# Optimization experiments

Measured on AMD Instinct MI355X. Metric: run time of the kernel, lower is better.

## Reference

```python
import jax, jax.numpy as jnp
import numpy as np

B, S, HID = 1, 4096, 768
NH, HD = 12, 64  # num heads, head dim


def setup_inputs() -> dict:
    key = jax.random.key(0)
    ks = jax.random.split(key, 7)
    scale = 1.0 / np.sqrt(HID)
    return {
        "hidden_states": jax.random.normal(ks[0], (B, S, HID), dtype=jnp.float32),
        "attention_mask": jnp.zeros((B, 1, 1, S), dtype=jnp.float32),
        "Wq": jax.random.normal(ks[1], (HID, HID), dtype=jnp.float32) * scale,
        "bq": jnp.zeros((HID,), dtype=jnp.float32),
        "Wk": jax.random.normal(ks[2], (HID, HID), dtype=jnp.float32) * scale,
        "bk": jnp.zeros((HID,), dtype=jnp.float32),
        "Wv": jax.random.normal(ks[3], (HID, HID), dtype=jnp.float32) * scale,
        "bv": jnp.zeros((HID,), dtype=jnp.float32),
    }


def _split_heads(x):
    # [B,S,HID] -> [B,NH,S,HD]
    b, s, _ = x.shape
    return x.reshape(b, s, NH, HD).transpose(0, 2, 1, 3)


def reference(hidden_states, attention_mask, Wq, bq, Wk, bk, Wv, bv):
    q = _split_heads(jnp.einsum('bsh,ho->bso', hidden_states, Wq) + bq)
    k = _split_heads(jnp.einsum('bsh,ho->bso', hidden_states, Wk) + bk)
    v = _split_heads(jnp.einsum('bsh,ho->bso', hidden_states, Wv) + bv)
    # attention scores: [B,NH,S,S]
    scores = jnp.einsum('bnqd,bnkd->bnqk', q, k) / np.sqrt(HD)
    scores = scores + attention_mask  # additive mask broadcast [B,1,1,S]
    probs = jax.nn.softmax(scores, axis=-1)
    ctx = jnp.einsum('bnqk,bnkd->bnqd', probs, v)
    # [B,NH,S,HD] -> [B,S,HID]
    b = ctx.shape[0]
    return ctx.transpose(0, 2, 1, 3).reshape(b, -1, NH * HD)
```

## Files before the change

### kernel.cpp

```cpp
#include <hip/hip_runtime.h>

typedef _Float16 f16;
typedef __attribute__((ext_vector_type(8))) _Float16 half8;
typedef __attribute__((ext_vector_type(4))) _Float16 half4;
typedef __attribute__((ext_vector_type(2))) _Float16 half2v;
typedef __attribute__((ext_vector_type(4))) float f32x4;

#define S_LEN 4096
#define HID   768
#define NH    12
#define HD    64

#define EXP2(x) __builtin_amdgcn_exp2f(x)
#define PKRTZ(a, b) __builtin_bit_cast(half2v, __builtin_amdgcn_cvt_pkrtz((a), (b)))

__global__ __launch_bounds__(256) void k_convert_x(const float* __restrict__ x,
                                                   f16* __restrict__ xb) {
  int i = blockIdx.x * 256 + threadIdx.x;
  float4 v = ((const float4*)x)[i];
  half4 h;
  h[0] = (f16)v.x; h[1] = (f16)v.y; h[2] = (f16)v.z; h[3] = (f16)v.w;
  *(half4*)&xb[(size_t)i * 4] = h;
}

__global__ __launch_bounds__(256) void k_maskcvt(const float* __restrict__ m,
                                                 float* __restrict__ m2) {
  int i = blockIdx.x * 256 + threadIdx.x;
  const float LOG2E = 1.4426950408889634f;
  float4 v = ((const float4*)m)[i];
  ((float4*)m2)[i] = make_float4(v.x * LOG2E, v.y * LOG2E, v.z * LOG2E, v.w * LOG2E);
}

__global__ __launch_bounds__(256) void k_transw(const float* __restrict__ Wq,
                                                const float* __restrict__ Wk,
                                                const float* __restrict__ Wv,
                                                f16* __restrict__ wtb) {
  __shared__ float tile[32][33];
  const float* W = (blockIdx.z == 0) ? Wq : (blockIdx.z == 1 ? Wk : Wv);
  f16* wt = wtb + (size_t)blockIdx.z * HID * HID;
  int k0 = blockIdx.y * 32, n0 = blockIdx.x * 32;
  int tx = threadIdx.x, ty = threadIdx.y;
  #pragma unroll
  for (int j = ty; j < 32; j += 8)
    tile[j][tx] = W[(size_t)(k0 + j) * HID + n0 + tx];
  __syncthreads();
  #pragma unroll
  for (int j = ty; j < 32; j += 8)
    wt[(size_t)(n0 + j) * HID + k0 + tx] = (f16)tile[tx][j];
}

__global__ __launch_bounds__(256) void k_gemm_qkv(const f16* __restrict__ xb,
                                                  const f16* __restrict__ wtb,
                                                  const float* __restrict__ bq,
                                                  const float* __restrict__ bk,
                                                  const float* __restrict__ bv,
                                                  f16* __restrict__ qo,
                                                  f16* __restrict__ ko,
                                                  f16* __restrict__ vto) {
  __shared__ __align__(16) f16 As[128 * 32];
  __shared__ __align__(16) f16 Bs[128 * 32];
  const int z = blockIdx.z;
  const f16* wt = wtb + (size_t)z * HID * HID;
  const float* bias = (z == 0) ? bq : (z == 1 ? bk : bv);
  const int brow = blockIdx.y * 128;
  const int bcol = blockIdx.x * 128;
  const int tid = threadIdx.x, wid = tid >> 6, lane = tid & 63;
  const int wr = wid >> 1, wc = wid & 1;
  const int lrow = lane & 15, lk8 = (lane >> 4) * 8;
  const int srow = lane >> 2;
  const int scol = (lane & 3) * 8;

  f32x4 acc[4][4] = {};

  for (int kt = 0; kt < HID; kt += 32) {
    #pragma unroll
    for (int r = 0; r < 2; r++) {
      int row = (wid * 2 + r) * 16 + srow;
      const f16* ga = xb + (size_t)(brow + row) * HID + kt + scol;
      const f16* gb = wt + (size_t)(bcol + row) * HID + kt + scol;
      __builtin_amdgcn_global_load_lds(
          (const __attribute__((address_space(1))) void*)ga,
          (__attribute__((address_space(3))) void*)(As + (wid * 2 + r) * 512),
          16, 0, 0);
      __builtin_amdgcn_global_load_lds(
          (const __attribute__((address_space(1))) void*)gb,
          (__attribute__((address_space(3))) void*)(Bs + (wid * 2 + r) * 512),
          16, 0, 0);
    }
    __syncthreads();

    half8 a[4], b[4];
    #pragma unroll
    for (int m = 0; m < 4; m++)
      a[m] = *(const half8*)&As[(wr * 64 + m * 16 + lrow) * 32 + lk8];
    #pragma unroll
    for (int n = 0; n < 4; n++)
      b[n] = *(const half8*)&Bs[(wc * 64 + n * 16 + lrow) * 32 + lk8];
    #pragma unroll
    for (int m = 0; m < 4; m++)
      #pragma unroll
      for (int n = 0; n < 4; n++)
        acc[m][n] = __builtin_amdgcn_mfma_f32_16x16x32_f16(a[m], b[n], acc[m][n], 0, 0, 0);
    __syncthreads();
  }

  #pragma unroll
  for (int m = 0; m < 4; m++) {
    int row0 = brow + wr * 64 + m * 16 + (lane >> 4) * 4;
    #pragma unroll
    for (int n = 0; n < 4; n++) {
      int col = bcol + wc * 64 + n * 16 + lrow;
      float bsv = bias[col];
      int h = col >> 6, d = col & 63;
      #pragma unroll
      for (int i = 0; i < 4; i++) {
        f16 v = (f16)(acc[m][n][i] + bsv);
        int r2 = row0 + i;
        if (z == 2)      vto[(size_t)(h * HD + d) * S_LEN + r2] = v;
        else if (z == 1) ko[((size_t)h * S_LEN + r2) * HD + d] = v;
        else             qo[((size_t)h * S_LEN + r2) * HD + d] = v;
      }
    }
  }
}

__global__ __launch_bounds__(256) void k_attn(const f16* __restrict__ qb,
                                              const f16* __restrict__ kb,
                                              const f16* __restrict__ vt,
                                              const float* __restrict__ mask2,
                                              float* __restrict__ out) {
  __shared__ __align__(16) f16 Ks[2][64 * 64];
  __shared__ __align__(16) f16 Vs[2][64 * 64];
  __shared__ __align__(16) f16 P[4][16 * 72];
  const int h = blockIdx.y;
  const int tid = threadIdx.x, wid = tid >> 6, lane = tid & 63;
  const int lrow = lane & 15, lk8 = (lane >> 4) * 8, g4 = (lane >> 4) * 4;
  const int grp = lane >> 4;
  const int qrow0 = blockIdx.x * 64 + wid * 16;
  const size_t hqk = (size_t)h * (S_LEN * HD);
  f16* Pw = &P[wid][0];
  const float LOG2E = 1.4426950408889634f;
  const float scale2 = 0.125f * LOG2E;

  const int srow = tid >> 3;
  const int sc   = tid & 7;

  const half8 aq0 = *(const half8*)&qb[hqk + (size_t)(qrow0 + lrow) * HD + lk8];
  const half8 aq1 = *(const half8*)&qb[hqk + (size_t)(qrow0 + lrow) * HD + 32 + lk8];

  f32x4 acc[4] = {};
  float mi = -INFINITY, li = 0.f;

  auto stage = [&](int buf, int kt) {
    #pragma unroll
    for (int r = 0; r < 2; r++) {
      const int row = r * 32 + srow;
      const int scol = ((sc ^ (row & 7)) << 3);
      const f16* gk = kb + hqk + (size_t)(kt + row) * HD + scol;
      const f16* gv = vt + ((size_t)(h * HD + row)) * S_LEN + kt + scol;
      f16* dk = &Ks[buf][r * 2048 + (tid << 3)];
      f16* dv = &Vs[buf][r * 2048 + (tid << 3)];
      __builtin_amdgcn_global_load_lds(
          (const __attribute__((address_space(1))) void*)gk,
          (__attribute__((address_space(3))) void*)dk, 16, 0, 0);
      __builtin_amdgcn_global_load_lds(
          (const __attribute__((address_space(1))) void*)gv,
          (__attribute__((address_space(3))) void*)dv, 16, 0, 0);
    }
  };

  stage(0, 0);
  __syncthreads();

  for (int it = 0; it < S_LEN / 64; ++it) {
    const int cur = it & 1;
    const int kt = it * 64;
    if (it + 1 < S_LEN / 64) stage(cur ^ 1, kt + 64);

    f32x4 sp[4];
    {
      half8 b0[4], b1[4];
      #pragma unroll
      for (int nt = 0; nt < 4; nt++) {
        const int row = nt * 16 + lrow;
        b0[nt] = *(const half8*)&Ks[cur][row * 64 + ((grp ^ (row & 7)) << 3)];
        b1[nt] = *(const half8*)&Ks[cur][row * 64 + (((4 + grp) ^ (row & 7)) << 3)];
      }
      __builtin_amdgcn_s_setprio(1);
      #pragma unroll
      for (int nt = 0; nt < 4; nt++) {
        f32x4 sv = {};
        sv = __builtin_amdgcn_mfma_f32_16x16x32_f16(b0[nt], aq0, sv, 0, 0, 0);
        sv = __builtin_amdgcn_mfma_f32_16x16x32_f16(b1[nt], aq1, sv, 0, 0, 0);
        sp[nt] = sv;
      }
      __builtin_amdgcn_s_setprio(0);
    }
    #pragma unroll
    for (int nt = 0; nt < 4; nt++) {
      float4 mk = *(const float4*)&mask2[kt + nt * 16 + g4];
      sp[nt][0] = sp[nt][0] * scale2 + mk.x;
      sp[nt][1] = sp[nt][1] * scale2 + mk.y;
      sp[nt][2] = sp[nt][2] * scale2 + mk.z;
      sp[nt][3] = sp[nt][3] * scale2 + mk.w;
    }
    float mloc = fmaxf(sp[0][0], sp[0][1]);
    mloc = fmaxf(fmaxf(mloc, sp[0][2]), sp[0][3]);
    mloc = fmaxf(fmaxf(mloc, sp[1][0]), sp[1][1]);
    mloc = fmaxf(fmaxf(mloc, sp[1][2]), sp[1][3]);
    mloc = fmaxf(fmaxf(mloc, sp[2][0]), sp[2][1]);
    mloc = fmaxf(fmaxf(mloc, sp[2][2]), sp[2][3]);
    mloc = fmaxf(fmaxf(mloc, sp[3][0]), sp[3][1]);
    mloc = fmaxf(fmaxf(mloc, sp[3][2]), sp[3][3]);
    mloc = fmaxf(mloc, __shfl_xor(mloc, 16, 64));
    mloc = fmaxf(mloc, __shfl_xor(mloc, 32, 64));

    float al = 1.f;
    if (!__all(mloc <= mi + 8.f)) {
      const float mn = fmaxf(mi, mloc);
      al = EXP2(mi - mn);
      mi = mn;
      #pragma unroll
      for (int nd = 0; nd < 4; nd++) {
        acc[nd][0] *= al; acc[nd][1] *= al; acc[nd][2] *= al; acc[nd][3] *= al;
      }
    }
    float rs = 0.f;
    #pragma unroll
    for (int nt = 0; nt < 4; nt++)
      #pragma unroll
      for (int i = 0; i < 4; i++) {
        sp[nt][i] = EXP2(sp[nt][i] - mi);
        rs += sp[nt][i];
      }
    rs += __shfl_xor(rs, 16, 64);
    rs += __shfl_xor(rs, 32, 64);
    li = li * al + rs;

    #pragma unroll
    for (int nt = 0; nt < 4; nt++) {
      half2v lo = PKRTZ(sp[nt][0], sp[nt][1]);
      half2v hi = PKRTZ(sp[nt][2], sp[nt][3]);
      half4 h4;
      h4[0] = lo[0]; h4[1] = lo[1]; h4[2] = hi[0]; h4[3] = hi[1];
      *(half4*)&Pw[lrow * 72 + nt * 16 + g4] = h4;
    }
    #pragma unroll
    for (int k2 = 0; k2 < 2; k2++) {
      half8 bp = *(const half8*)&Pw[lrow * 72 + k2 * 32 + lk8];
      __builtin_amdgcn_s_setprio(1);
      #pragma unroll
      for (int nd = 0; nd < 4; nd++) {
        const int vr = nd * 16 + lrow;
        const int xc = (((k2 * 4 + grp) ^ (vr & 7)) << 3);
        half8 av = *(const half8*)&Vs[cur][vr * 64 + xc];
        acc[nd] = __builtin_amdgcn_mfma_f32_16x16x32_f16(av, bp, acc[nd], 0, 0, 0);
      }
      __builtin_amdgcn_s_setprio(0);
    }
    __syncthreads();
  }

  const float inv = (li > 0.f) ? (1.f / li) : 0.f;
  #pragma unroll
  for (int nd = 0; nd < 4; nd++) {
    float4 o = make_float4(acc[nd][0] * inv, acc[nd][1] * inv,
                           acc[nd][2] * inv, acc[nd][3] * inv);
    *(float4*)&out[(size_t)(qrow0 + lrow) * HID + h * HD + nd * 16 + g4] = o;
  }
}

extern "C" void kernel_launch(void* const* d_in, const int* in_sizes, int n_in,
                              void* d_out, int out_size, void* d_ws, size_t ws_size,
                              hipStream_t stream) {
  const float* x    = (const float*)d_in[0];
  const float* mask = (const float*)d_in[1];
  const float* Wq   = (const float*)d_in[2];
  const float* bq   = (const float*)d_in[3];
  const float* Wk   = (const float*)d_in[4];
  const float* bk   = (const float*)d_in[5];
  const float* Wv   = (const float*)d_in[6];
  const float* bv   = (const float*)d_in[7];
  float* out = (float*)d_out;

  char* ws = (char*)d_ws;
  f16* xb  = (f16*)(ws);
  f16* wtb = (f16*)(ws + 6291456);
  f16* qbb = (f16*)(ws + 9830400);
  f16* kbb = (f16*)(ws + 16121856);
  f16* vtb = (f16*)(ws + 22413312);
  float* mask2 = (float*)ws;

  k_convert_x<<<dim3(3072), dim3(256), 0, stream>>>(x, xb);
  k_transw<<<dim3(24, 24, 3), dim3(32, 8), 0, stream>>>(Wq, Wk, Wv, wtb);
  k_gemm_qkv<<<dim3(6, 32, 3), dim3(256), 0, stream>>>(xb, wtb, bq, bk, bv, qbb, kbb, vtb);
  k_maskcvt<<<dim3(4), dim3(256), 0, stream>>>(mask, mask2);
  k_attn<<<dim3(64, NH), dim3(256), 0, stream>>>(qbb, kbb, vtb, mask2, out);
}
```

Before: 149.2 us.

## Rewrite attention with 32x32 MFMA, register P via permlane swap, split-K waves

```diff
diff --git a/kernel.cpp b/kernel.cpp
--- a/kernel.cpp
+++ b/kernel.cpp
@@ -3,8 +3,9 @@
 typedef _Float16 f16;
 typedef __attribute__((ext_vector_type(8))) _Float16 half8;
 typedef __attribute__((ext_vector_type(4))) _Float16 half4;
-typedef __attribute__((ext_vector_type(2))) _Float16 half2v;
 typedef __attribute__((ext_vector_type(4))) float f32x4;
+typedef __attribute__((ext_vector_type(16))) float f32x16;
+typedef __attribute__((ext_vector_type(4))) unsigned u32x4;
 
 #define S_LEN 4096
 #define HID   768
@@ -12,7 +13,22 @@
 #define HD    64
 
 #define EXP2(x) __builtin_amdgcn_exp2f(x)
-#define PKRTZ(a, b) __builtin_bit_cast(half2v, __builtin_amdgcn_cvt_pkrtz((a), (b)))
+#define PKRTZ_U(a, b) __builtin_bit_cast(unsigned, __builtin_amdgcn_cvt_pkrtz((a), (b)))
+
+__device__ inline void lane32swap(unsigned &x, unsigned &y) {
+#if __has_builtin(__builtin_amdgcn_permlane32_swap)
+  auto r = __builtin_amdgcn_permlane32_swap((int)x, (int)y, false, false);
+  x = (unsigned)r[0];
+  y = (unsigned)r[1];
+#else
+  unsigned px = (unsigned)__shfl_xor((int)x, 32, 64);
+  unsigned py = (unsigned)__shfl_xor((int)y, 32, 64);
+  bool hi = (threadIdx.x & 32) != 0;
+  unsigned nx = hi ? py : x;
+  unsigned ny = hi ? y : px;
+  x = nx; y = ny;
+#endif
+}
 
 __global__ __launch_bounds__(256) void k_convert_x(const float* __restrict__ x,
                                                    f16* __restrict__ xb) {
@@ -124,95 +140,102 @@
   }
 }
 
-__global__ __launch_bounds__(256) void k_attn(const f16* __restrict__ qb,
-                                              const f16* __restrict__ kb,
-                                              const f16* __restrict__ vt,
-                                              const float* __restrict__ mask2,
-                                              float* __restrict__ out) {
+__global__ __launch_bounds__(256, 3) void k_attn(const f16* __restrict__ qb,
+                                                 const f16* __restrict__ kb,
+                                                 const f16* __restrict__ vt,
+                                                 const float* __restrict__ mask2,
+                                                 float* __restrict__ out) {
   __shared__ __align__(16) f16 Ks[2][64 * 64];
-  __shared__ __align__(16) f16 Vs[2][64 * 64];
-  __shared__ __align__(16) f16 P[4][16 * 72];
+  __shared__ float cml[2][2][64];
   const int h = blockIdx.y;
   const int tid = threadIdx.x, wid = tid >> 6, lane = tid & 63;
-  const int lrow = lane & 15, lk8 = (lane >> 4) * 8, g4 = (lane >> 4) * 4;
-  const int grp = lane >> 4;
-  const int qrow0 = blockIdx.x * 64 + wid * 16;
+  const int q31 = lane & 31, lh = lane >> 5;
+  const int qset = wid >> 1, par = wid & 1;
+  const int qrow0 = blockIdx.x * 64 + qset * 32;
   const size_t hqk = (size_t)h * (S_LEN * HD);
-  f16* Pw = &P[wid][0];
-  const float LOG2E = 1.4426950408889634f;
-  const float scale2 = 0.125f * LOG2E;
-
-  const int srow = tid >> 3;
-  const int sc   = tid & 7;
-
-  const half8 aq0 = *(const half8*)&qb[hqk + (size_t)(qrow0 + lrow) * HD + lk8];
-  const half8 aq1 = *(const half8*)&qb[hqk + (size_t)(qrow0 + lrow) * HD + 32 + lk8];
-
-  f32x4 acc[4] = {};
+  const float scale2 = 0.125f * 1.4426950408889634f;
+
+  half8 aq[4];
+  #pragma unroll
+  for (int kdc = 0; kdc < 4; kdc++)
+    aq[kdc] = *(const half8*)&qb[hqk + (size_t)(qrow0 + q31) * HD + kdc * 16 + lh * 8];
+
+  const f16* vb0 = vt + ((size_t)(h * HD) + q31) * S_LEN + lh * 8;
+  const f16* vb1 = vb0 + (size_t)32 * S_LEN;
+
+  f32x16 acc0 = {}, acc1 = {};
   float mi = -INFINITY, li = 0.f;
 
-  auto stage = [&](int buf, int kt) {
-    #pragma unroll
-    for (int r = 0; r < 2; r++) {
-      const int row = r * 32 + srow;
-      const int scol = ((sc ^ (row & 7)) << 3);
-      const f16* gk = kb + hqk + (size_t)(kt + row) * HD + scol;
-      const f16* gv = vt + ((size_t)(h * HD + row)) * S_LEN + kt + scol;
-      f16* dk = &Ks[buf][r * 2048 + (tid << 3)];
-      f16* dv = &Vs[buf][r * 2048 + (tid << 3)];
-      __builtin_amdgcn_global_load_lds(
-          (const __attribute__((address_space(1))) void*)gk,
-          (__attribute__((address_space(3))) void*)dk, 16, 0, 0);
-      __builtin_amdgcn_global_load_lds(
-          (const __attribute__((address_space(1))) void*)gv,
-          (__attribute__((address_space(3))) void*)dv, 16, 0, 0);
-    }
+  const int srow0 = (wid * 2) * 8 + (lane >> 3);
+  const int srow1 = (wid * 2 + 1) * 8 + (lane >> 3);
+  const int sc0 = ((lane & 7) ^ (srow0 & 7)) * 8;
+  const int sc1 = ((lane & 7) ^ (srow1 & 7)) * 8;
+
+  auto stage = [&](int b, int tt) {
+    const f16* g0 = kb + hqk + (size_t)(tt * 64 + srow0) * HD + sc0;
+    const f16* g1 = kb + hqk + (size_t)(tt * 64 + srow1) * HD + sc1;
+    __builtin_amdgcn_global_load_lds(
+        (const __attribute__((address_space(1))) void*)g0,
+        (__attribute__((address_space(3))) void*)&Ks[b][(wid * 2) * 512 + lane * 8], 16, 0, 0);
+    __builtin_amdgcn_global_load_lds(
+        (const __attribute__((address_space(1))) void*)g1,
+        (__attribute__((address_space(3))) void*)&Ks[b][(wid * 2 + 1) * 512 + lane * 8], 16, 0, 0);
   };
 
   stage(0, 0);
+  stage(1, 1);
   __syncthreads();
 
-  for (int it = 0; it < S_LEN / 64; ++it) {
-    const int cur = it & 1;
-    const int kt = it * 64;
-    if (it + 1 < S_LEN / 64) stage(cur ^ 1, kt + 64);
-
-    f32x4 sp[4];
-    {
-      half8 b0[4], b1[4];
-      #pragma unroll
-      for (int nt = 0; nt < 4; nt++) {
-        const int row = nt * 16 + lrow;
-        b0[nt] = *(const half8*)&Ks[cur][row * 64 + ((grp ^ (row & 7)) << 3)];
-        b1[nt] = *(const half8*)&Ks[cur][row * 64 + (((4 + grp) ^ (row & 7)) << 3)];
-      }
-      __builtin_amdgcn_s_setprio(1);
-      #pragma unroll
-      for (int nt = 0; nt < 4; nt++) {
-        f32x4 sv = {};
-        sv = __builtin_amdgcn_mfma_f32_16x16x32_f16(b0[nt], aq0, sv, 0, 0, 0);
-        sv = __builtin_amdgcn_mfma_f32_16x16x32_f16(b1[nt], aq1, sv, 0, 0, 0);
-        sp[nt] = sv;
-      }
-      __builtin_amdgcn_s_setprio(0);
-    }
-    #pragma unroll
-    for (int nt = 0; nt < 4; nt++) {
-      float4 mk = *(const float4*)&mask2[kt + nt * 16 + g4];
-      sp[nt][0] = sp[nt][0] * scale2 + mk.x;
-      sp[nt][1] = sp[nt][1] * scale2 + mk.y;
-      sp[nt][2] = sp[nt][2] * scale2 + mk.z;
-      sp[nt][3] = sp[nt][3] * scale2 + mk.w;
-    }
-    float mloc = fmaxf(sp[0][0], sp[0][1]);
-    mloc = fmaxf(fmaxf(mloc, sp[0][2]), sp[0][3]);
-    mloc = fmaxf(fmaxf(mloc, sp[1][0]), sp[1][1]);
-    mloc = fmaxf(fmaxf(mloc, sp[1][2]), sp[1][3]);
-    mloc = fmaxf(fmaxf(mloc, sp[2][0]), sp[2][1]);
-    mloc = fmaxf(fmaxf(mloc, sp[2][2]), sp[2][3]);
-    mloc = fmaxf(fmaxf(mloc, sp[3][0]), sp[3][1]);
-    mloc = fmaxf(fmaxf(mloc, sp[3][2]), sp[3][3]);
-    mloc = fmaxf(mloc, __shfl_xor(mloc, 16, 64));
+  for (int d = 0; d < 32; ++d) {
+    const int kt = (2 * d + par) * 64;
+
+    half8 kf[2][4];
+    #pragma unroll
+    for (int T = 0; T < 2; T++)
+      #pragma unroll
+      for (int kdc = 0; kdc < 4; kdc++)
+        kf[T][kdc] = *(const half8*)&Ks[par][(T * 32 + q31) * 64 +
+                                             (((kdc * 2 + lh) ^ (q31 & 7)) * 8)];
+    __syncthreads();
+
+    if (d < 31) { stage(0, 2 * d + 2); stage(1, 2 * d + 3); }
+
+    half8 vf0[4];
+    #pragma unroll
+    for (int kc = 0; kc < 4; kc++) vf0[kc] = *(const half8*)(vb0 + kt + kc * 16);
+
+    f32x16 s0 = {}, s1 = {};
+    __builtin_amdgcn_s_setprio(1);
+    #pragma unroll
+    for (int kdc = 0; kdc < 4; kdc++)
+      s0 = __builtin_amdgcn_mfma_f32_32x32x16_f16(kf[0][kdc], aq[kdc], s0, 0, 0, 0);
+    #pragma unroll
+    for (int kdc = 0; kdc < 4; kdc++)
+      s1 = __builtin_amdgcn_mfma_f32_32x32x16_f16(kf[1][kdc], aq[kdc], s1, 0, 0, 0);
+    __builtin_amdgcn_s_setprio(0);
+
+    half8 vf1[4];
+    #pragma unroll
+    for (int kc = 0; kc < 4; kc++) vf1[kc] = *(const half8*)(vb1 + kt + kc * 16);
+
+    #pragma unroll
+    for (int m = 0; m < 4; m++) {
+      float4 mk0 = *(const float4*)&mask2[kt + 8 * m + 4 * lh];
+      float4 mk1 = *(const float4*)&mask2[kt + 32 + 8 * m + 4 * lh];
+      s0[4 * m + 0] = s0[4 * m + 0] * scale2 + mk0.x;
+      s0[4 * m + 1] = s0[4 * m + 1] * scale2 + mk0.y;
+      s0[4 * m + 2] = s0[4 * m + 2] * scale2 + mk0.z;
+      s0[4 * m + 3] = s0[4 * m + 3] * scale2 + mk0.w;
+      s1[4 * m + 0] = s1[4 * m + 0] * scale2 + mk1.x;
+      s1[4 * m + 1] = s1[4 * m + 1] * scale2 + mk1.y;
+      s1[4 * m + 2] = s1[4 * m + 2] * scale2 + mk1.z;
+      s1[4 * m + 3] = s1[4 * m + 3] * scale2 + mk1.w;
+    }
+    float mloc = fmaxf(s0[0], s0[1]);
+    #pragma unroll
+    for (int i = 2; i < 16; i++) mloc = fmaxf(mloc, s0[i]);
+    #pragma unroll
+    for (int i = 0; i < 16; i++) mloc = fmaxf(mloc, s1[i]);
     mloc = fmaxf(mloc, __shfl_xor(mloc, 32, 64));
 
     float al = 1.f;
@@ -221,52 +244,92 @@
       al = EXP2(mi - mn);
       mi = mn;
       #pragma unroll
-      for (int nd = 0; nd < 4; nd++) {
-        acc[nd][0] *= al; acc[nd][1] *= al; acc[nd][2] *= al; acc[nd][3] *= al;
-      }
+      for (int i = 0; i < 16; i++) { acc0[i] *= al; acc1[i] *= al; }
     }
     float rs = 0.f;
     #pragma unroll
-    for (int nt = 0; nt < 4; nt++)
-      #pragma unroll
-      for (int i = 0; i < 4; i++) {
-        sp[nt][i] = EXP2(sp[nt][i] - mi);
-        rs += sp[nt][i];
-      }
-    rs += __shfl_xor(rs, 16, 64);
+    for (int i = 0; i < 16; i++) { s0[i] = EXP2(s0[i] - mi); rs += s0[i]; }
+    #pragma unroll
+    for (int i = 0; i < 16; i++) { s1[i] = EXP2(s1[i] - mi); rs += s1[i]; }
     rs += __shfl_xor(rs, 32, 64);
     li = li * al + rs;
 
-    #pragma unroll
-    for (int nt = 0; nt < 4; nt++) {
-      half2v lo = PKRTZ(sp[nt][0], sp[nt][1]);
-      half2v hi = PKRTZ(sp[nt][2], sp[nt][3]);
-      half4 h4;
-      h4[0] = lo[0]; h4[1] = lo[1]; h4[2] = hi[0]; h4[3] = hi[1];
-      *(half4*)&Pw[lrow * 72 + nt * 16 + g4] = h4;
-    }
-    #pragma unroll
-    for (int k2 = 0; k2 < 2; k2++) {
-      half8 bp = *(const half8*)&Pw[lrow * 72 + k2 * 32 + lk8];
-      __builtin_amdgcn_s_setprio(1);
-      #pragma unroll
-      for (int nd = 0; nd < 4; nd++) {
-        const int vr = nd * 16 + lrow;
-        const int xc = (((k2 * 4 + grp) ^ (vr & 7)) << 3);
-        half8 av = *(const half8*)&Vs[cur][vr * 64 + xc];
-        acc[nd] = __builtin_amdgcn_mfma_f32_16x16x32_f16(av, bp, acc[nd], 0, 0, 0);
+    half8 pf[4];
+    #pragma unroll
+    for (int T = 0; T < 2; T++) {
+      unsigned a0[4], a1[4];
+      #pragma unroll
+      for (int m = 0; m < 4; m++) {
+        if (T == 0) {
+          a0[m] = PKRTZ_U(s0[4 * m + 0], s0[4 * m + 1]);
+          a1[m] = PKRTZ_U(s0[4 * m + 2], s0[4 * m + 3]);
+        } else {
+          a0[m] = PKRTZ_U(s1[4 * m + 0], s1[4 * m + 1]);
+          a1[m] = PKRTZ_U(s1[4 * m + 2], s1[4 * m + 3]);
+        }
       }
-      __builtin_amdgcn_s_setprio(0);
-    }
+      #pragma unroll
+      for (int c = 0; c < 2; c++) {
+        unsigned w0 = a0[2 * c], w2 = a0[2 * c + 1];
+        unsigned w1 = a1[2 * c], w3 = a1[2 * c + 1];
+        lane32swap(w0, w2);
+        lane32swap(w1, w3);
+        u32x4 t;
+        t[0] = w0; t[1] = w1; t[2] = w2; t[3] = w3;
+        pf[2 * T + c] = __builtin_bit_cast(half8, t);
+      }
+    }
+
+    __builtin_amdgcn_s_setprio(1);
+    #pragma unroll
+    for (int kc = 0; kc < 4; kc++)
+      acc0 = __builtin_amdgcn_mfma_f32_32x32x16_f16(vf0[kc], pf[kc], acc0, 0, 0, 0);
+    #pragma unroll
+    for (int kc = 0; kc < 4; kc++)
+      acc1 = __builtin_amdgcn_mfma_f32_32x32x16_f16(vf1[kc], pf[kc], acc1, 0, 0, 0);
+    __builtin_amdgcn_s_setprio(0);
+
     __syncthreads();
   }
 
-  const float inv = (li > 0.f) ? (1.f / li) : 0.f;
-  #pragma unroll
-  for (int nd = 0; nd < 4; nd++) {
-    float4 o = make_float4(acc[nd][0] * inv, acc[nd][1] * inv,
-                           acc[nd][2] * inv, acc[nd][3] * inv);
-    *(float4*)&out[(size_t)(qrow0 + lrow) * HID + h * HD + nd * 16 + g4] = o;
+  float* cacc = (float*)&Ks[0][0];
+  if (par == 1) {
+    float* dst = cacc + qset * 2048;
+    #pragma unroll
+    for (int i = 0; i < 16; i++) {
+      dst[i * 64 + lane] = acc0[i];
+      dst[(16 + i) * 64 + lane] = acc1[i];
+    }
+    cml[qset][0][lane] = mi;
+    cml[qset][1][lane] = li;
+  }
+  __syncthreads();
+  if (par == 0) {
+    const float mo = cml[qset][0][lane], lo2 = cml[qset][1][lane];
+    const float* src = cacc + qset * 2048;
+    const float M = fmaxf(mi, mo);
+    const float we = EXP2(mi - M), wo = EXP2(mo - M);
+    const float l = li * we + lo2 * wo;
+    const float inv = (l > 0.f) ? 1.f / l : 0.f;
+    float* orow = out + (size_t)(qrow0 + q31) * HID + h * HD;
+    #pragma unroll
+    for (int m = 0; m < 4; m++) {
+      float4 v;
+      v.x = (acc0[4 * m + 0] * we + src[(4 * m + 0) * 64 + lane] * wo) * inv;
+      v.y = (acc0[4 * m + 1] * we + src[(4 * m + 1) * 64 + lane] * wo) * inv;
+      v.z = (acc0[4 * m + 2] * we + src[(4 * m + 2) * 64 + lane] * wo) * inv;
+      v.w = (acc0[4 * m + 3] * we + src[(4 * m + 3) * 64 + lane] * wo) * inv;
+      *(float4*)&orow[8 * m + 4 * lh] = v;
+    }
+    #pragma unroll
+    for (int m = 0; m < 4; m++) {
+      float4 v;
+      v.x = (acc1[4 * m + 0] * we + src[(16 + 4 * m + 0) * 64 + lane] * wo) * inv;
+      v.y = (acc1[4 * m + 1] * we + src[(16 + 4 * m + 1) * 64 + lane] * wo) * inv;
+      v.z = (acc1[4 * m + 2] * we + src[(16 + 4 * m + 2) * 64 + lane] * wo) * inv;
+      v.w = (acc1[4 * m + 3] * we + src[(16 + 4 * m + 3) * 64 + lane] * wo) * inv;
+      *(float4*)&orow[32 + 8 * m + 4 * lh] = v;
+    }
   }
 }
 
```

Result: slower. 186.8 us (+25.2%).

## Split attention over key range, read V from global, add combine kernel

Applied to the files above, without the earlier changes.

```diff
diff --git a/kernel.cpp b/kernel.cpp
--- a/kernel.cpp
+++ b/kernel.cpp
@@ -124,23 +124,24 @@
   }
 }
 
-__global__ __launch_bounds__(256) void k_attn(const f16* __restrict__ qb,
-                                              const f16* __restrict__ kb,
-                                              const f16* __restrict__ vt,
-                                              const float* __restrict__ mask2,
-                                              float* __restrict__ out) {
+__global__ __launch_bounds__(256, 5) void k_attn(const f16* __restrict__ qb,
+                                                 const f16* __restrict__ kb,
+                                                 const f16* __restrict__ vt,
+                                                 const float* __restrict__ mask2,
+                                                 float* __restrict__ dsto,
+                                                 float* __restrict__ ml,
+                                                 int nkt, int direct) {
   __shared__ __align__(16) f16 Ks[2][64 * 64];
-  __shared__ __align__(16) f16 Vs[2][64 * 64];
   __shared__ __align__(16) f16 P[4][16 * 72];
-  const int h = blockIdx.y;
+  const int h = blockIdx.y, z = blockIdx.z;
   const int tid = threadIdx.x, wid = tid >> 6, lane = tid & 63;
   const int lrow = lane & 15, lk8 = (lane >> 4) * 8, g4 = (lane >> 4) * 4;
   const int grp = lane >> 4;
   const int qrow0 = blockIdx.x * 64 + wid * 16;
   const size_t hqk = (size_t)h * (S_LEN * HD);
+  const int kt0 = z * nkt * 64;
   f16* Pw = &P[wid][0];
-  const float LOG2E = 1.4426950408889634f;
-  const float scale2 = 0.125f * LOG2E;
+  const float scale2 = 0.125f * 1.4426950408889634f;
 
   const int srow = tid >> 3;
   const int sc   = tid & 7;
@@ -157,25 +158,28 @@
       const int row = r * 32 + srow;
       const int scol = ((sc ^ (row & 7)) << 3);
       const f16* gk = kb + hqk + (size_t)(kt + row) * HD + scol;
-      const f16* gv = vt + ((size_t)(h * HD + row)) * S_LEN + kt + scol;
-      f16* dk = &Ks[buf][r * 2048 + (tid << 3)];
-      f16* dv = &Vs[buf][r * 2048 + (tid << 3)];
       __builtin_amdgcn_global_load_lds(
           (const __attribute__((address_space(1))) void*)gk,
-          (__attribute__((address_space(3))) void*)dk, 16, 0, 0);
-      __builtin_amdgcn_global_load_lds(
-          (const __attribute__((address_space(1))) void*)gv,
-          (__attribute__((address_space(3))) void*)dv, 16, 0, 0);
+          (__attribute__((address_space(3))) void*)&Ks[buf][r * 2048 + (tid << 3)],
+          16, 0, 0);
     }
   };
 
-  stage(0, 0);
+  stage(0, kt0);
   __syncthreads();
 
-  for (int it = 0; it < S_LEN / 64; ++it) {
+  for (int it = 0; it < nkt; ++it) {
     const int cur = it & 1;
-    const int kt = it * 64;
-    if (it + 1 < S_LEN / 64) stage(cur ^ 1, kt + 64);
+    const int kt = kt0 + it * 64;
+    if (it + 1 < nkt) stage(cur ^ 1, kt + 64);
+
+    half8 vf[2][4];
+    #pragma unroll
+    for (int k2 = 0; k2 < 2; k2++)
+      #pragma unroll
+      for (int nd = 0; nd < 4; nd++)
+        vf[k2][nd] = *(const half8*)&vt[((size_t)(h * HD + nd * 16 + lrow)) * S_LEN +
+                                        kt + k2 * 32 + lk8];
 
     f32x4 sp[4];
     {
@@ -250,24 +254,61 @@
       half8 bp = *(const half8*)&Pw[lrow * 72 + k2 * 32 + lk8];
       __builtin_amdgcn_s_setprio(1);
       #pragma unroll
-      for (int nd = 0; nd < 4; nd++) {
-        const int vr = nd * 16 + lrow;
-        const int xc = (((k2 * 4 + grp) ^ (vr & 7)) << 3);
-        half8 av = *(const half8*)&Vs[cur][vr * 64 + xc];
-        acc[nd] = __builtin_amdgcn_mfma_f32_16x16x32_f16(av, bp, acc[nd], 0, 0, 0);
-      }
+      for (int nd = 0; nd < 4; nd++)
+        acc[nd] = __builtin_amdgcn_mfma_f32_16x16x32_f16(vf[k2][nd], bp, acc[nd], 0, 0, 0);
       __builtin_amdgcn_s_setprio(0);
     }
     __syncthreads();
   }
 
   const float inv = (li > 0.f) ? (1.f / li) : 0.f;
-  #pragma unroll
-  for (int nd = 0; nd < 4; nd++) {
-    float4 o = make_float4(acc[nd][0] * inv, acc[nd][1] * inv,
-                           acc[nd][2] * inv, acc[nd][3] * inv);
-    *(float4*)&out[(size_t)(qrow0 + lrow) * HID + h * HD + nd * 16 + g4] = o;
-  }
+  if (direct) {
+    #pragma unroll
+    for (int nd = 0; nd < 4; nd++) {
+      float4 o = make_float4(acc[nd][0] * inv, acc[nd][1] * inv,
+                             acc[nd][2] * inv, acc[nd][3] * inv);
+      *(float4*)&dsto[(size_t)(qrow0 + lrow) * HID + h * HD + nd * 16 + g4] = o;
+    }
+  } else {
+    const size_t rbase = ((size_t)z * NH + h) * S_LEN + qrow0 + lrow;
+    #pragma unroll
+    for (int nd = 0; nd < 4; nd++) {
+      float4 o = make_float4(acc[nd][0] * inv, acc[nd][1] * inv,
+                             acc[nd][2] * inv, acc[nd][3] * inv);
+      *(float4*)&dsto[rbase * HD + nd * 16 + g4] = o;
+    }
+    if (lane < 16) {
+      ml[rbase * 2]     = mi;
+      ml[rbase * 2 + 1] = li;
+    }
+  }
+}
+
+__global__ __launch_bounds__(256) void k_combine(const float* __restrict__ opart,
+                                                 const float* __restrict__ ml,
+                                                 float* __restrict__ out, int split) {
+  const int gid = blockIdx.x * 256 + threadIdx.x;
+  const int row = gid >> 4;
+  const int d0 = (gid & 15) << 2;
+  const int h = row >> 12, q = row & (S_LEN - 1);
+  float M = -INFINITY;
+  for (int zz = 0; zz < split; zz++)
+    M = fmaxf(M, ml[((size_t)zz * NH * S_LEN + row) * 2]);
+  float wsum = 0.f;
+  float o0 = 0.f, o1 = 0.f, o2 = 0.f, o3 = 0.f;
+  for (int zz = 0; zz < split; zz++) {
+    const size_t r = (size_t)zz * NH * S_LEN + row;
+    float m = ml[r * 2], l = ml[r * 2 + 1];
+    if (l > 0.f) {
+      float w = l * EXP2(m - M);
+      float4 v = *(const float4*)&opart[r * HD + d0];
+      wsum += w;
+      o0 += w * v.x; o1 += w * v.y; o2 += w * v.z; o3 += w * v.w;
+    }
+  }
+  const float inv = (wsum > 0.f) ? (1.f / wsum) : 0.f;
+  *(float4*)&out[(size_t)q * HID + h * HD + d0] =
+      make_float4(o0 * inv, o1 * inv, o2 * inv, o3 * inv);
 }
 
 extern "C" void kernel_launch(void* const* d_in, const int* in_sizes, int n_in,
@@ -291,9 +332,25 @@
   f16* vtb = (f16*)(ws + 22413312);
   float* mask2 = (float*)ws;
 
+  const size_t base   = 28704768;
+  const size_t o_per  = (size_t)NH * S_LEN * HD * 4;
+  const size_t ml_per = (size_t)NH * S_LEN * 2 * 4;
+
+  int split = (ws_size >= base + 2 * (o_per + ml_per)) ? 2 : 1;
+
   k_convert_x<<<dim3(3072), dim3(256), 0, stream>>>(x, xb);
   k_transw<<<dim3(24, 24, 3), dim3(32, 8), 0, stream>>>(Wq, Wk, Wv, wtb);
   k_gemm_qkv<<<dim3(6, 32, 3), dim3(256), 0, stream>>>(xb, wtb, bq, bk, bv, qbb, kbb, vtb);
   k_maskcvt<<<dim3(4), dim3(256), 0, stream>>>(mask, mask2);
-  k_attn<<<dim3(64, NH), dim3(256), 0, stream>>>(qbb, kbb, vtb, mask2, out);
-}
+
+  if (split == 1) {
+    k_attn<<<dim3(64, NH, 1), dim3(256), 0, stream>>>(qbb, kbb, vtb, mask2, out, out,
+                                                      S_LEN / 64, 1);
+  } else {
+    float* opart = (float*)(ws + base);
+    float* mlb   = (float*)(ws + base + (size_t)split * o_per);
+    k_attn<<<dim3(64, NH, split), dim3(256), 0, stream>>>(qbb, kbb, vtb, mask2, opart, mlb,
+                                                          S_LEN / (64 * split), 0);
+    k_combine<<<dim3(NH * S_LEN * 16 / 256), dim3(256), 0, stream>>>(opart, mlb, out, split);
+  }
+}
```

After: 371.2 us. 2.49x slower.
